# Performance work log

Hardware: AMD Instinct MI355X
Metric: run time of the kernel (lower is better)

Reference implementation:

```python
import jax, jax.numpy as jnp
import numpy as np

MASS = 0.5
G = 1.0  # constant offset -p[8]*g in the objective; does not affect argmin u*
NEWTON_ITERS = 30


def _lambertw(x):
    """Solve w*exp(w) = x for x >= 0 (principal branch) via Newton iterations."""
    w = jnp.log1p(x)  # good init on [0, inf)
    for _ in range(NEWTON_ITERS):
        ew = jnp.exp(w)
        w = w - (w * ew - x) / (ew * (w + 1.0))
    return w


def setup_inputs() -> dict:
    key = jax.random.key(0)
    kz, kt, k1, k2 = jax.random.split(key, 4)
    B, S, H = 500000, 12, 100
    return {
        "z": jax.random.normal(kz, (B, S), jnp.float32),
        "t": jax.random.uniform(kt, (B,), jnp.float32),
        "W1": jax.random.normal(k1, (S + 1, H), jnp.float32) * 0.1,
        "b1": jnp.zeros((H,), jnp.float32),
        "W2": jax.random.normal(k2, (H, S), jnp.float32) * 0.1,
        "b2": jnp.zeros((S,), jnp.float32),
    }


def reference(z, t, W1, b1, W2, b2):
    # p_net: MLP on concat([t, z])
    inp = jnp.concatenate([t[:, None], z], axis=1)          # [B, 13]
    h = jnp.tanh(inp @ W1 + b1)                              # [B, 100]
    p = h @ W2 + b2                                          # [B, 12]
    # Objective: c . u + exp(0.5*||u||^2) + const, with
    # c = [(p6+p7+p8)/m, p9, p10, p11]. Stationarity: c + u*exp(0.5||u||^2)=0
    # => u = -c*exp(-0.5*w), where w = ||u||^2 solves w*e^w = ||c||^2 (Lambert W).
    c = jnp.stack(
        [(p[:, 6] + p[:, 7] + p[:, 8]) / MASS, p[:, 9], p[:, 10], p[:, 11]],
        axis=1,
    )                                                        # [B, 4]
    x = jnp.sum(c * c, axis=1)                               # [B] = ||c||^2
    w = _lambertw(x)                                         # [B]
    ustar = -c * jnp.exp(-0.5 * w)[:, None]                  # [B, 4]
    return ustar
```

## Files before the change

### kernel.cpp

```cpp
#include <hip/hip_runtime.h>


constexpr int S = 12;
constexpr int H = 100;
#define TWO_LOG2E 2.8853900817779268f

typedef float vf2 __attribute__((ext_vector_type(2)));

__device__ __forceinline__ float fast_rcp(float x) {
    return __builtin_amdgcn_rcpf(x);
}

__global__ __launch_bounds__(256) void pack_weights(
    const float* __restrict__ W1, const float* __restrict__ b1,
    const float* __restrict__ W2, float* __restrict__ ws)
{
    int idx = blockIdx.x * 256 + threadIdx.x;
    if (idx < 1600) {
        int jp = idx >> 5, s = idx & 31;
        float v = 0.0f;
        if (s < 26) {
            int k = s >> 1, half = s & 1;
            v = W1[k * H + 2 * jp + half] * TWO_LOG2E;
        } else if (s < 28) {
            int half = s & 1;
            v = b1[2 * jp + half] * TWO_LOG2E;
        }
        ws[idx] = v;
    } else if (idx < 2400) {
        int r = idx - 1600;
        int jp = r >> 4, s = r & 15;
        float v = 0.0f;
        if (s < 12) {
            int m = s >> 1, half = s & 1;
            v = W2[(2 * jp + half) * S + 6 + m];
        }
        ws[idx] = v;
    }
}

__global__ __launch_bounds__(256) void cvx_quad_kernel(
    const float* __restrict__ z, const float* __restrict__ t,
    const float* __restrict__ ws, const float* __restrict__ b2,
    float* __restrict__ out, int B)
{
    int tid = blockIdx.x * 256 + threadIdx.x;
    if (tid >= B) return;

    float inp[S + 1];
    inp[0] = t[tid];
    const float4* zr = reinterpret_cast<const float4*>(z) + (size_t)tid * 3;
    float4 a0 = zr[0], a1 = zr[1], a2 = zr[2];
    inp[1]  = a0.x; inp[2]  = a0.y; inp[3]  = a0.z; inp[4]  = a0.w;
    inp[5]  = a1.x; inp[6]  = a1.y; inp[7]  = a1.z; inp[8]  = a1.w;
    inp[9]  = a2.x; inp[10] = a2.y; inp[11] = a2.z; inp[12] = a2.w;

    vf2 pA[6];
    #pragma unroll
    for (int m = 0; m < 6; ++m) {
        pA[m] = (vf2){b2[6 + m], 0.0f};
    }

    #pragma unroll 2
    for (int jp = 0; jp < H / 2; ++jp) {
        const vf2* wrow = reinterpret_cast<const vf2*>(ws + jp * 32);
        vf2 acc = wrow[13];
        #pragma unroll
        for (int k = 0; k < S + 1; ++k) {
            acc = __builtin_elementwise_fma((vf2){inp[k], inp[k]}, wrow[k], acc);
        }

        float e0 = __builtin_amdgcn_exp2f(acc.x);
        float e1 = __builtin_amdgcn_exp2f(acc.y);
        vf2 ab = (vf2){e0, e1} + (vf2){1.0f, 1.0f};
        float r = fast_rcp(ab.x * ab.y);
        vf2 inv = (vf2){ab.y, ab.x} * (vf2){r, r};
        vf2 th = __builtin_elementwise_fma((vf2){-2.0f, -2.0f}, inv,
                                           (vf2){1.0f, 1.0f});

        const vf2* qrow = reinterpret_cast<const vf2*>(ws + 1600 + jp * 16);
        #pragma unroll
        for (int m = 0; m < 6; ++m) {
            pA[m] = __builtin_elementwise_fma(th, qrow[m], pA[m]);
        }
    }

    float p0 = pA[0].x + pA[0].y, p1 = pA[1].x + pA[1].y, p2 = pA[2].x + pA[2].y;
    float p3 = pA[3].x + pA[3].y, p4 = pA[4].x + pA[4].y, p5 = pA[5].x + pA[5].y;

    float c0 = 2.0f * (p0 + p1 + p2);
    float c1 = p3, c2 = p4, c3 = p5;
    float x = fmaf(c0, c0, fmaf(c1, c1, fmaf(c2, c2, c3 * c3)));

    float w = __logf(1.0f + x);
    #pragma unroll
    for (int it = 0; it < 5; ++it) {
        float ew  = __expf(w);
        float num = fmaf(w, ew, -x);
        float den = fmaf(ew, w, ew);
        w = w - num * fast_rcp(den);
    }

    float sc = -__expf(-0.5f * w);
    float4 o;
    o.x = c0 * sc;
    o.y = c1 * sc;
    o.z = c2 * sc;
    o.w = c3 * sc;
    reinterpret_cast<float4*>(out)[tid] = o;
}

extern "C" void kernel_launch(void* const* d_in, const int* in_sizes, int n_in,
                              void* d_out, int out_size, void* d_ws, size_t ws_size,
                              hipStream_t stream) {
    const float* z  = (const float*)d_in[0];
    const float* t  = (const float*)d_in[1];
    const float* W1 = (const float*)d_in[2];
    const float* b1 = (const float*)d_in[3];
    const float* W2 = (const float*)d_in[4];
    const float* b2 = (const float*)d_in[5];
    float* out = (float*)d_out;
    float* ws  = (float*)d_ws;

    pack_weights<<<dim3(10), dim3(256), 0, stream>>>(W1, b1, W2, ws);

    int B = in_sizes[1];
    int grid = (B + 255) / 256;
    cvx_quad_kernel<<<dim3(grid), dim3(256), 0, stream>>>(z, t, ws, b2, out, B);
}
```

Before: 107.1 us.

## Compute MLP layers with split-bf16 MFMA and persistent per-wave tiling

Replaces the per-thread scalar FMA MLP with 16-row tiles per wavefront. Both layers run as bf16 MFMA 16x16x32 using a hi/lo split (three products) to approximate fp32 accuracy, with weights prepacked into MFMA fragment layout and held in registers. Tanh outputs are staged through LDS to form the second-layer A operand, and each wave loops over several tiles while prefetching the next input tile. The aim is to move the dominant FMA work onto the matrix cores. In exchange it adds LDS round trips, split/convert ALU work, and a Lambert-W epilogue that runs on only 16 of 64 lanes, and the dropped lo*lo term slightly reduces precision.

```diff
diff --git a/kernel.cpp b/kernel.cpp
--- a/kernel.cpp
+++ b/kernel.cpp
@@ -5,10 +5,26 @@
 constexpr int H = 100;
 #define TWO_LOG2E 2.8853900817779268f
 
-typedef float vf2 __attribute__((ext_vector_type(2)));
+typedef float f32x4 __attribute__((ext_vector_type(4)));
+typedef __bf16 bf16x8 __attribute__((ext_vector_type(8)));
+typedef unsigned int uint4v __attribute__((ext_vector_type(4)));
+
+struct HiLo { unsigned h, l; };
 
 __device__ __forceinline__ float fast_rcp(float x) {
     return __builtin_amdgcn_rcpf(x);
+}
+
+__device__ __forceinline__ HiLo split2(float f0, float f1) {
+    unsigned b0 = __float_as_uint(f0), b1 = __float_as_uint(f1);
+    float h0 = __uint_as_float(b0 & 0xffff0000u);
+    float h1 = __uint_as_float(b1 & 0xffff0000u);
+    unsigned l0 = __float_as_uint(f0 - h0) >> 16;
+    unsigned l1 = __float_as_uint(f1 - h1) >> 16;
+    HiLo r;
+    r.h = (b0 >> 16) | (b1 & 0xffff0000u);
+    r.l = l0 | (l1 << 16);
+    return r;
 }
 
 __global__ __launch_bounds__(256) void pack_weights(
@@ -16,98 +32,199 @@
     const float* __restrict__ W2, float* __restrict__ ws)
 {
     int idx = blockIdx.x * 256 + threadIdx.x;
-    if (idx < 1600) {
-        int jp = idx >> 5, s = idx & 31;
-        float v = 0.0f;
-        if (s < 26) {
-            int k = s >> 1, half = s & 1;
-            v = W1[k * H + 2 * jp + half] * TWO_LOG2E;
-        } else if (s < 28) {
-            int half = s & 1;
-            v = b1[2 * jp + half] * TWO_LOG2E;
-        }
-        ws[idx] = v;
-    } else if (idx < 2400) {
-        int r = idx - 1600;
-        int jp = r >> 4, s = r & 15;
-        float v = 0.0f;
-        if (s < 12) {
-            int m = s >> 1, half = s & 1;
-            v = W2[(2 * jp + half) * S + 6 + m];
-        }
-        ws[idx] = v;
-    }
+    if (idx >= 5632) return;
+    unsigned halves[2];
+    if (idx < 3584) {
+        int d = idx & 3, lane = (idx >> 2) & 63, tp = idx >> 8;
+        int t = tp >> 1, p = tp & 1;
+        int g = lane >> 4, n = (t << 4) + (lane & 15);
+        #pragma unroll
+        for (int h = 0; h < 2; ++h) {
+            int k = g * 8 + 2 * d + h;
+            float f = 0.0f;
+            if (n < H) {
+                if (k < 13)       f = W1[k * H + n];
+                else if (k == 13) f = b1[n];
+            }
+            unsigned bb = __float_as_uint(f);
+            unsigned hb = bb >> 16;
+            float hf = __uint_as_float(bb & 0xffff0000u);
+            unsigned lb = __float_as_uint(f - hf) >> 16;
+            halves[h] = p ? lb : hb;
+        }
+    } else {
+        int r = idx - 3584;
+        int d = r & 3, lane = (r >> 2) & 63, sp = r >> 8;
+        int s = sp >> 1, p = sp & 1;
+        int g = lane >> 4, c = lane & 15;
+        #pragma unroll
+        for (int h = 0; h < 2; ++h) {
+            int k = s * 32 + g * 8 + 2 * d + h;
+            float f = (k < H && c < 6) ? W2[k * S + 6 + c] : 0.0f;
+            unsigned bb = __float_as_uint(f);
+            unsigned hb = bb >> 16;
+            float hf = __uint_as_float(bb & 0xffff0000u);
+            unsigned lb = __float_as_uint(f - hf) >> 16;
+            halves[h] = p ? lb : hb;
+        }
+    }
+    reinterpret_cast<unsigned*>(ws)[idx] = halves[0] | (halves[1] << 16);
 }
 
 __global__ __launch_bounds__(256) void cvx_quad_kernel(
     const float* __restrict__ z, const float* __restrict__ t,
     const float* __restrict__ ws, const float* __restrict__ b2,
-    float* __restrict__ out, int B)
+    float* __restrict__ out, int B, int ntiles, int tpw)
 {
-    int tid = blockIdx.x * 256 + threadIdx.x;
-    if (tid >= B) return;
-
-    float inp[S + 1];
-    inp[0] = t[tid];
-    const float4* zr = reinterpret_cast<const float4*>(z) + (size_t)tid * 3;
-    float4 a0 = zr[0], a1 = zr[1], a2 = zr[2];
-    inp[1]  = a0.x; inp[2]  = a0.y; inp[3]  = a0.z; inp[4]  = a0.w;
-    inp[5]  = a1.x; inp[6]  = a1.y; inp[7]  = a1.z; inp[8]  = a1.w;
-    inp[9]  = a2.x; inp[10] = a2.y; inp[11] = a2.z; inp[12] = a2.w;
-
-    vf2 pA[6];
+    __shared__ float lds[4 * 2240];
+    int lane = threadIdx.x & 63;
+    int wid  = threadIdx.x >> 6;
+    float* wbase = lds + wid * 2240;
+    float* pbase = wbase + 16 * 132;
+    int g = lane >> 4, c15 = lane & 15;
+
+    int gw = blockIdx.x * 4 + wid;
+    int t0 = gw * tpw;
+    if (t0 >= ntiles) return;
+    int tend = t0 + tpw; if (tend > ntiles) tend = ntiles;
+
+    const uint4v* wsv = reinterpret_cast<const uint4v*>(ws);
+    uint4v b1f[7][2], b2f[4][2];
     #pragma unroll
-    for (int m = 0; m < 6; ++m) {
-        pA[m] = (vf2){b2[6 + m], 0.0f};
-    }
-
-    #pragma unroll 2
-    for (int jp = 0; jp < H / 2; ++jp) {
-        const vf2* wrow = reinterpret_cast<const vf2*>(ws + jp * 32);
-        vf2 acc = wrow[13];
-        #pragma unroll
-        for (int k = 0; k < S + 1; ++k) {
-            acc = __builtin_elementwise_fma((vf2){inp[k], inp[k]}, wrow[k], acc);
-        }
-
-        float e0 = __builtin_amdgcn_exp2f(acc.x);
-        float e1 = __builtin_amdgcn_exp2f(acc.y);
-        vf2 ab = (vf2){e0, e1} + (vf2){1.0f, 1.0f};
-        float r = fast_rcp(ab.x * ab.y);
-        vf2 inv = (vf2){ab.y, ab.x} * (vf2){r, r};
-        vf2 th = __builtin_elementwise_fma((vf2){-2.0f, -2.0f}, inv,
-                                           (vf2){1.0f, 1.0f});
-
-        const vf2* qrow = reinterpret_cast<const vf2*>(ws + 1600 + jp * 16);
-        #pragma unroll
-        for (int m = 0; m < 6; ++m) {
-            pA[m] = __builtin_elementwise_fma(th, qrow[m], pA[m]);
-        }
-    }
-
-    float p0 = pA[0].x + pA[0].y, p1 = pA[1].x + pA[1].y, p2 = pA[2].x + pA[2].y;
-    float p3 = pA[3].x + pA[3].y, p4 = pA[4].x + pA[4].y, p5 = pA[5].x + pA[5].y;
-
-    float c0 = 2.0f * (p0 + p1 + p2);
-    float c1 = p3, c2 = p4, c3 = p5;
-    float x = fmaf(c0, c0, fmaf(c1, c1, fmaf(c2, c2, c3 * c3)));
-
-    float w = __logf(1.0f + x);
+    for (int tt = 0; tt < 7; ++tt) {
+        b1f[tt][0] = wsv[(tt * 2 + 0) * 64 + lane];
+        b1f[tt][1] = wsv[(tt * 2 + 1) * 64 + lane];
+    }
     #pragma unroll
-    for (int it = 0; it < 5; ++it) {
-        float ew  = __expf(w);
-        float num = fmaf(w, ew, -x);
-        float den = fmaf(ew, w, ew);
-        w = w - num * fast_rcp(den);
-    }
-
-    float sc = -__expf(-0.5f * w);
-    float4 o;
-    o.x = c0 * sc;
-    o.y = c1 * sc;
-    o.z = c2 * sc;
-    o.w = c3 * sc;
-    reinterpret_cast<float4*>(out)[tid] = o;
+    for (int s = 0; s < 4; ++s) {
+        b2f[s][0] = wsv[896 + (s * 2 + 0) * 64 + lane];
+        b2f[s][1] = wsv[896 + (s * 2 + 1) * 64 + lane];
+    }
+    float bb[6];
+    #pragma unroll
+    for (int c = 0; c < 6; ++c) bb[c] = b2[6 + c];
+
+    {
+        int i = lane * 4, m = i >> 4, c = i & 15;
+        float4 zz; zz.x = 0.f; zz.y = 0.f; zz.z = 0.f; zz.w = 0.f;
+        *reinterpret_cast<float4*>(wbase + m * 132 + 112 + c) = zz;
+    }
+
+    auto LOADX = [&](int tile, float xv[8]) {
+        int row = tile * 16 + c15; if (row >= B) row = B - 1;
+        const float* zr = z + (size_t)row * 12;
+        if (g == 0) {
+            float4 za = *reinterpret_cast<const float4*>(zr);
+            float2 zb = *reinterpret_cast<const float2*>(zr + 4);
+            float  zc = zr[6];
+            xv[0] = t[row]; xv[1] = za.x; xv[2] = za.y; xv[3] = za.z;
+            xv[4] = za.w;   xv[5] = zb.x; xv[6] = zb.y; xv[7] = zc;
+        } else if (g == 1) {
+            float  zd = zr[7];
+            float4 ze = *reinterpret_cast<const float4*>(zr + 8);
+            xv[0] = zd;   xv[1] = ze.x; xv[2] = ze.y; xv[3] = ze.z;
+            xv[4] = ze.w; xv[5] = 1.0f; xv[6] = 0.0f; xv[7] = 0.0f;
+        } else {
+            #pragma unroll
+            for (int i2 = 0; i2 < 8; ++i2) xv[i2] = 0.0f;
+        }
+    };
+
+    float xcur[8];
+    LOADX(t0, xcur);
+
+    for (int tt = t0; tt < tend; ++tt) {
+        uint4v ah, al;
+        {
+            HiLo r0 = split2(xcur[0], xcur[1]);
+            HiLo r1 = split2(xcur[2], xcur[3]);
+            HiLo r2 = split2(xcur[4], xcur[5]);
+            HiLo r3 = split2(xcur[6], xcur[7]);
+            ah.x = r0.h; al.x = r0.l;
+            ah.y = r1.h; al.y = r1.l;
+            ah.z = r2.h; al.z = r2.l;
+            ah.w = r3.h; al.w = r3.l;
+        }
+        if (tt + 1 < tend) LOADX(tt + 1, xcur);
+
+        bf16x8 A1h = __builtin_bit_cast(bf16x8, ah);
+        bf16x8 A1l = __builtin_bit_cast(bf16x8, al);
+
+        #pragma unroll
+        for (int nt = 0; nt < 7; ++nt) {
+            f32x4 acc = {0.f, 0.f, 0.f, 0.f};
+            bf16x8 Bh = __builtin_bit_cast(bf16x8, b1f[nt][0]);
+            bf16x8 Bl = __builtin_bit_cast(bf16x8, b1f[nt][1]);
+            acc = __builtin_amdgcn_mfma_f32_16x16x32_bf16(A1h, Bh, acc, 0, 0, 0);
+            acc = __builtin_amdgcn_mfma_f32_16x16x32_bf16(A1h, Bl, acc, 0, 0, 0);
+            acc = __builtin_amdgcn_mfma_f32_16x16x32_bf16(A1l, Bh, acc, 0, 0, 0);
+            #pragma unroll
+            for (int r = 0; r < 4; ++r) {
+                float e  = __builtin_amdgcn_exp2f(acc[r] * TWO_LOG2E);
+                float th = fmaf(-2.0f, fast_rcp(e + 1.0f), 1.0f);
+                wbase[(g * 4 + r) * 132 + nt * 16 + c15] = th;
+            }
+        }
+
+        f32x4 p = {0.f, 0.f, 0.f, 0.f};
+        #pragma unroll
+        for (int s = 0; s < 4; ++s) {
+            const float* src = wbase + c15 * 132 + s * 32 + g * 8;
+            float4 v0 = *reinterpret_cast<const float4*>(src);
+            float4 v1 = *reinterpret_cast<const float4*>(src + 4);
+            uint4v a2h, a2l;
+            {
+                HiLo r0 = split2(v0.x, v0.y);
+                HiLo r1 = split2(v0.z, v0.w);
+                HiLo r2 = split2(v1.x, v1.y);
+                HiLo r3 = split2(v1.z, v1.w);
+                a2h.x = r0.h; a2l.x = r0.l;
+                a2h.y = r1.h; a2l.y = r1.l;
+                a2h.z = r2.h; a2l.z = r2.l;
+                a2h.w = r3.h; a2l.w = r3.l;
+            }
+            bf16x8 A2h = __builtin_bit_cast(bf16x8, a2h);
+            bf16x8 A2l = __builtin_bit_cast(bf16x8, a2l);
+            bf16x8 Bh = __builtin_bit_cast(bf16x8, b2f[s][0]);
+            bf16x8 Bl = __builtin_bit_cast(bf16x8, b2f[s][1]);
+            p = __builtin_amdgcn_mfma_f32_16x16x32_bf16(A2h, Bh, p, 0, 0, 0);
+            p = __builtin_amdgcn_mfma_f32_16x16x32_bf16(A2h, Bl, p, 0, 0, 0);
+            p = __builtin_amdgcn_mfma_f32_16x16x32_bf16(A2l, Bh, p, 0, 0, 0);
+        }
+
+        if (c15 < 6) {
+            #pragma unroll
+            for (int r = 0; r < 4; ++r) pbase[(g * 4 + r) * 8 + c15] = p[r];
+        }
+
+        if (lane < 16) {
+            int m = lane;
+            float4 pa = *reinterpret_cast<const float4*>(pbase + m * 8);
+            float2 pb = *reinterpret_cast<const float2*>(pbase + m * 8 + 4);
+            float p0 = pa.x + bb[0], p1 = pa.y + bb[1], p2 = pa.z + bb[2];
+            float p3 = pa.w + bb[3], p4 = pb.x + bb[4], p5 = pb.y + bb[5];
+
+            float c0 = 2.0f * (p0 + p1 + p2);
+            float x = fmaf(c0, c0, fmaf(p3, p3, fmaf(p4, p4, p5 * p5)));
+
+            float w = __logf(1.0f + x);
+            #pragma unroll
+            for (int it = 0; it < 5; ++it) {
+                float ew  = __expf(w);
+                float num = fmaf(w, ew, -x);
+                float den = fmaf(ew, w, ew);
+                w = w - num * fast_rcp(den);
+            }
+            float sc = -__expf(-0.5f * w);
+
+            int row = tt * 16 + m;
+            if (row < B) {
+                float4 o;
+                o.x = c0 * sc; o.y = p3 * sc; o.z = p4 * sc; o.w = p5 * sc;
+                *reinterpret_cast<float4*>(out + (size_t)row * 4) = o;
+            }
+        }
+    }
 }
 
 extern "C" void kernel_launch(void* const* d_in, const int* in_sizes, int n_in,
@@ -122,9 +239,13 @@
     float* out = (float*)d_out;
     float* ws  = (float*)d_ws;
 
-    pack_weights<<<dim3(10), dim3(256), 0, stream>>>(W1, b1, W2, ws);
+    pack_weights<<<dim3(22), dim3(256), 0, stream>>>(W1, b1, W2, ws);
 
     int B = in_sizes[1];
-    int grid = (B + 255) / 256;
-    cvx_quad_kernel<<<dim3(grid), dim3(256), 0, stream>>>(z, t, ws, b2, out, B);
-}
+    int ntiles = (B + 15) / 16;
+    int tpw = (ntiles + 3124) / 3125;
+    int nwaves = (ntiles + tpw - 1) / tpw;
+    int grid = (nwaves + 3) / 4;
+    cvx_quad_kernel<<<dim3(grid), dim3(256), 0, stream>>>(
+        z, t, ws, b2, out, B, ntiles, tpw);
+}
```

Result: slower. 122.4 us (+14.3%).
